# Kernel optimization log

Measured on AMD Instinct MI355X. Metric: run time of the kernel, lower is better.

## Reference

```python
import jax, jax.numpy as jnp
import numpy as np

NC = 4
X = Y = Z = 64
IMG_SHAPE = (96, 96, 96)
SPAN = 2          # FILTER_SIZE = [5,5,5]
NUM_ITER = 4
DIL = 2           # DILATION = 2.0
SMOOTH_DISTANCE_INIT = 0.3
PRIOR_DISTANCE_INIT = 0.3


def _ind(d):
    # mirrors _get_ind from the torch code
    return (d, 0) if d > 0 else (0, -d)


def _sl(a, b):
    # slice(a, -b) with -0 -> None, mirrors _negative
    return slice(a, -b if b else None)


def _offsets():
    for dx in range(-SPAN, SPAN + 1):
        for dy in range(-SPAN, SPAN + 1):
            for dz in range(-SPAN, SPAN + 1):
                yield dx, dy, dz


def _lin_resize_axis(x, axis, out):
    # 1D linear interpolation matching torch align_corners=True
    n = x.shape[axis]
    if out == n:
        return x
    pos = jnp.arange(out, dtype=x.dtype) * ((n - 1) / (out - 1))
    i0 = jnp.clip(jnp.floor(pos).astype(jnp.int32), 0, n - 1)
    i1 = jnp.clip(i0 + 1, 0, n - 1)
    w = pos - i0.astype(x.dtype)
    shp = [1] * x.ndim
    shp[axis] = out
    w = w.reshape(shp)
    return jnp.take(x, i0, axis=axis) * (1 - w) + jnp.take(x, i1, axis=axis) * w


def _resize3d(x, out_sz):
    # trilinear, align_corners=True, separable over the 3 spatial axes of [b,c,X,Y,Z]
    for ax, o in zip((2, 3, 4), out_sz):
        x = _lin_resize_axis(x, ax, o)
    return x


def _smooth_gaussian(feats):
    # feats: [b, c, X, Y, Z] -> gaussian [b, 5,5,5, X, Y, Z]
    b = feats.shape[0]
    sp = feats.shape[2:]
    g = jnp.zeros((b, 5, 5, 5) + sp, feats.dtype)
    for dx, dy, dz in _offsets():
        dx1, dx2 = _ind(dx); dy1, dy2 = _ind(dy); dz1, dz2 = _ind(dz)
        a = feats[:, :, _sl(dx1, dx2), _sl(dy1, dy2), _sl(dz1, dz2)]
        c = feats[:, :, _sl(dx2, dx1), _sl(dy2, dy1), _sl(dz2, dz1)]
        e = jnp.exp(-0.5 * jnp.sum((a - c) ** 2, axis=1))
        g = g.at[:, dx + SPAN, dy + SPAN, dz + SPAN,
                 _sl(dx2, dx1), _sl(dy2, dy1), _sl(dz2, dz1)].set(e)
    return g


def _prior_gaussian(f1, f2):
    # f1, f2: [b, c, x, y, z] (already downsampled) -> [b, 5,5,5, x, y, z]
    b = f1.shape[0]
    sp = f1.shape[2:]
    g = jnp.zeros((b, 5, 5, 5) + sp, f1.dtype)
    for dx, dy, dz in _offsets():
        dx1, dx2 = _ind(dx); dy1, dy2 = _ind(dy); dz1, dz2 = _ind(dz)
        a = f1[:, :, _sl(dx2, dx1), _sl(dy2, dy1), _sl(dz2, dz1)]
        c = f2[:, :, _sl(dx1, dx2), _sl(dy1, dy2), _sl(dz1, dz2)]
        e = jnp.exp(-0.5 * jnp.sum((a - c) ** 2, axis=1))
        g = g.at[:, dx + SPAN, dy + SPAN, dz + SPAN,
                 _sl(dx2, dx1), _sl(dy2, dy1), _sl(dz2, dz1)].set(e)
    return g


def _message(p, g):
    # p: [b, nc, x, y, z]; g: [b, 5,5,5, x, y, z]
    out = jnp.zeros_like(p)
    for dx, dy, dz in _offsets():
        dx1, dx2 = _ind(dx); dy1, dy2 = _ind(dy); dz1, dz2 = _ind(dz)
        a = p[:, :, _sl(dx1, dx2), _sl(dy1, dy2), _sl(dz1, dz2)]
        w = g[:, None, dx + SPAN, dy + SPAN, dz + SPAN,
              _sl(dx2, dx1), _sl(dy2, dy1), _sl(dz2, dz1)]
        out = out.at[:, :, _sl(dx2, dx1), _sl(dy2, dy1), _sl(dz2, dz1)].add(a * w)
    return out


def setup_inputs() -> dict:
    key = jax.random.key(0)
    ks = jax.random.split(key, 6)
    unary = jax.random.normal(ks[0], (1, NC, X, Y, Z), jnp.float32)
    img = jax.random.normal(ks[1], (1, 2, X, Y, Z), jnp.float32)
    atlas = jax.random.normal(ks[2], (1, 2, X, Y, Z), jnp.float32)
    atlas_label = jax.random.uniform(ks[3], (1, X, Y, Z, NC), jnp.float32)
    patch_start = jax.random.randint(ks[4], (1, 3), 0, 32, jnp.int32)
    return {
        "unary": unary,
        "img": img,
        "atlas": atlas,
        "atlas_label": atlas_label,
        "patch_start": patch_start,
        "smooth_norm": jnp.array([1.0 / SMOOTH_DISTANCE_INIT], jnp.float32),
        "smooth_weight": jnp.ones((NC,), jnp.float32),
        "prior_norm": jnp.array([1.0 / PRIOR_DISTANCE_INIT], jnp.float32),
        "prior_weight": jnp.ones(IMG_SHAPE, jnp.float32),
        "compat_w": jnp.eye(NC, dtype=jnp.float32),
    }


def reference(unary, img, atlas, atlas_label, patch_start,
              smooth_norm, smooth_weight, prior_norm, prior_weight, compat_w):
    b, nc, x, y, z = unary.shape
    ds = (x // DIL, y // DIL, z // DIL)  # floor(in*0.5) == ceil(in/2) for even dims

    # similarity kernels
    sg = _smooth_gaussian(img * smooth_norm)                      # [b,5,5,5,x,y,z]
    f1 = _resize3d(img * prior_norm, ds)
    f2 = _resize3d(atlas * prior_norm, ds)
    pg = _prior_gaussian(f1, f2)                                  # [b,5,5,5,x/2,y/2,z/2]

    # prior message is independent of q_values: compute once
    al = jnp.transpose(atlas_label, (0, 4, 1, 2, 3))              # [b,nc,x,y,z]
    al_ds = _resize3d(al, ds)
    pm = _resize3d(_message(al_ds, pg), (x, y, z))                # [b,nc,x,y,z]
    pw = jax.lax.dynamic_slice(
        prior_weight,
        (patch_start[0, 0], patch_start[0, 1], patch_start[0, 2]),
        (x, y, z))
    prior_term = pw[None, None] * pm

    q = unary
    for _ in range(NUM_ITER):
        p = jax.nn.softmax(q, axis=1)
        sm = _message(p, sg)
        pred = smooth_weight[None, :, None, None, None] * sm + prior_term
        q = unary + jnp.einsum('oc,bcxyz->boxyz', compat_w, pred)  # 1x1x1 compat conv
    return q
```

## Files before the change

### kernel.cpp

```cpp
#include <hip/hip_runtime.h>

#define NN 64
#define N3 (64*64*64)
#define DS 32

#define LOG2E 1.4426950408889634f
#define FSCALE 0.8493218002880191f

typedef _Float16 h2  __attribute__((ext_vector_type(2)));
typedef __fp16   h2f __attribute__((ext_vector_type(2)));

__device__ __forceinline__ float fexp2(float x) { return __builtin_amdgcn_exp2f(x); }

__device__ __forceinline__ h2 u2h(unsigned u) { union { unsigned u; h2 h; } c; c.u = u; return c.h; }
__device__ __forceinline__ unsigned h2u(h2 h) { union { unsigned u; h2 h; } c; c.h = h; return c.u; }
__device__ __forceinline__ h2 pkh(float a, float b) {
    union { h2f a; h2 b; } c; c.a = __builtin_amdgcn_cvt_pkrtz(a, b); return c.b;
}
__device__ __forceinline__ float fdot2(h2 a, h2 b) {
    union { h2 h; h2f f; } ca, cb; ca.h = a; cb.h = b;
    return __builtin_amdgcn_fdot2(ca.f, cb.f, 0.0f, false);
}


#define PMX 6
#define PMY 10
#define PMZ 10
#define SXD 10
#define SYD 14
#define SZD 14

__global__ __launch_bounds__(1024) void k_prior(
    const float* __restrict__ img, const float* __restrict__ atlas,
    const float* __restrict__ alabel, const float* __restrict__ unary,
    const float* __restrict__ pnorm, const float* __restrict__ snorm,
    const float* __restrict__ pweight, const int* __restrict__ pstart,
    const float* __restrict__ compat,
    float4* __restrict__ unary4, unsigned* __restrict__ fpk)
{
    __shared__ __align__(16) uint4 nbS[SXD][SYD][SZD];
    __shared__ __align__(8)  uint2 pmS[PMX][PMY][PMZ];

    const int tid = threadIdx.x;
    const int x0 = blockIdx.z * 8, y0 = blockIdx.y * 16, z0 = blockIdx.x * 16;
    const int cxlo = (x0*31)/63, cylo = (y0*31)/63, czlo = (z0*31)/63;

    const float pnf = pnorm[0] * FSCALE;
    const float sc  = snorm[0] * FSCALE;

    for (int i = tid; i < 8*16*16; i += 1024) {
        int fz = i & 15, fy = (i >> 4) & 15, fx = i >> 8;
        int g = ((x0+fx)*NN + (y0+fy))*NN + (z0+fz);
        fpk[g] = h2u(pkh(img[g]*sc, img[g+N3]*sc));
    }

    for (int i = tid; i < SXD*SYD*SZD; i += 1024) {
        int lz = i % SZD; int r = i / SZD; int ly = r % SYD; int lx = r / SYD;
        int cx = cxlo - 2 + lx, cy = cylo - 2 + ly, cz = czlo - 2 + lz;
        uint4 v = make_uint4(0u, 0u, 0u, 0u);
        if ((unsigned)cx < DS && (unsigned)cy < DS && (unsigned)cz < DS) {
            const float scale = 63.0f / 31.0f;
            float posx = cx*scale; int a0i = (int)posx; float wx = posx - a0i; int a1i = a0i+1 <= 63 ? a0i+1 : 63;
            float posy = cy*scale; int b0i = (int)posy; float wy = posy - b0i; int b1i = b0i+1 <= 63 ? b0i+1 : 63;
            float posz = cz*scale; int d0i = (int)posz; float wz = posz - d0i; int d1i = d0i+1 <= 63 ? d0i+1 : 63;
            float w000=(1-wx)*(1-wy)*(1-wz), w001=(1-wx)*(1-wy)*wz;
            float w010=(1-wx)*wy*(1-wz),     w011=(1-wx)*wy*wz;
            float w100=wx*(1-wy)*(1-wz),     w101=wx*(1-wy)*wz;
            float w110=wx*wy*(1-wz),         w111=wx*wy*wz;
            int c000=(a0i*NN+b0i)*NN+d0i, c001=(a0i*NN+b0i)*NN+d1i;
            int c010=(a0i*NN+b1i)*NN+d0i, c011=(a0i*NN+b1i)*NN+d1i;
            int c100=(a1i*NN+b0i)*NN+d0i, c101=(a1i*NN+b0i)*NN+d1i;
            int c110=(a1i*NN+b1i)*NN+d0i, c111=(a1i*NN+b1i)*NN+d1i;
            auto tri = [&](const float* p) -> float {
                return p[c000]*w000 + p[c001]*w001 + p[c010]*w010 + p[c011]*w011
                     + p[c100]*w100 + p[c101]*w101 + p[c110]*w110 + p[c111]*w111;
            };
            const float4* lab = (const float4*)alabel;
            float4 l = make_float4(0.f,0.f,0.f,0.f);
            {
                float4 t;
                t = lab[c000]; l.x += w000*t.x; l.y += w000*t.y; l.z += w000*t.z; l.w += w000*t.w;
                t = lab[c001]; l.x += w001*t.x; l.y += w001*t.y; l.z += w001*t.z; l.w += w001*t.w;
                t = lab[c010]; l.x += w010*t.x; l.y += w010*t.y; l.z += w010*t.z; l.w += w010*t.w;
                t = lab[c011]; l.x += w011*t.x; l.y += w011*t.y; l.z += w011*t.z; l.w += w011*t.w;
                t = lab[c100]; l.x += w100*t.x; l.y += w100*t.y; l.z += w100*t.z; l.w += w100*t.w;
                t = lab[c101]; l.x += w101*t.x; l.y += w101*t.y; l.z += w101*t.z; l.w += w101*t.w;
                t = lab[c110]; l.x += w110*t.x; l.y += w110*t.y; l.z += w110*t.z; l.w += w110*t.w;
                t = lab[c111]; l.x += w111*t.x; l.y += w111*t.y; l.z += w111*t.z; l.w += w111*t.w;
            }
            v = make_uint4(h2u(pkh(pnf*tri(atlas), pnf*tri(atlas + N3))),
                           h2u(pkh(l.x, l.y)), h2u(pkh(l.z, l.w)),
                           h2u(pkh(pnf*tri(img), pnf*tri(img + N3))));
        }
        nbS[lx][ly][lz] = v;
    }
    __syncthreads();

    for (int i = tid; i < PMX*PMY*PMZ; i += 1024) {
        int pz = i % PMZ; int r = i / PMZ; int py = r % PMY; int px = r / PMY;
        int cx = cxlo + px, cy = cylo + py, cz = czlo + pz;
        uint2 o = make_uint2(0u, 0u);
        if (cx < DS && cy < DS && cz < DS) {
            h2 ncf = -u2h(nbS[px+2][py+2][pz+2].w);
            float a0=0.f, a1=0.f, a2=0.f, a3=0.f;
            for (int dx = -2; dx <= 2; ++dx) {
                int xx = cx + dx; if ((unsigned)xx >= DS) continue;
                for (int dy = -2; dy <= 2; ++dy) {
                    int yy = cy + dy; if ((unsigned)yy >= DS) continue;
                    #pragma unroll
                    for (int dz = -2; dz <= 2; ++dz) {
                        int zz = cz + dz; if ((unsigned)zz >= DS) continue;
                        uint4 v = nbS[px+2+dx][py+2+dy][pz+2+dz];
                        h2 d = u2h(v.x) + ncf;
                        float w = fexp2(-fdot2(d, d));
                        h2 l01 = u2h(v.y), l23 = u2h(v.z);
                        a0 += w*(float)l01.x; a1 += w*(float)l01.y;
                        a2 += w*(float)l23.x; a3 += w*(float)l23.y;
                    }
                }
            }
            o = make_uint2(h2u(pkh(a0, a1)), h2u(pkh(a2, a3)));
        }
        pmS[px][py][pz] = o;
    }
    __syncthreads();

    const int ps0 = pstart[0], ps1 = pstart[1], ps2 = pstart[2];
    float cw[16];
    #pragma unroll
    for (int k = 0; k < 16; ++k) cw[k] = compat[k];
    const float S13 = 31.0f / 63.0f;

    for (int i = tid; i < 8*16*16; i += 1024) {
        int fz = i & 15, fy = (i >> 4) & 15, fx = i >> 8;
        int gx = x0 + fx, gy = y0 + fy, gz = z0 + fz;
        float posx = gx*S13; int xc0 = (int)posx; float wx = posx - xc0; int xc1 = xc0 < 31 ? xc0+1 : 31;
        float posy = gy*S13; int yc0 = (int)posy; float wy = posy - yc0; int yc1 = yc0 < 31 ? yc0+1 : 31;
        float posz = gz*S13; int zc0 = (int)posz; float wz = posz - zc0; int zc1 = zc0 < 31 ? zc0+1 : 31;
        int lx0 = xc0-cxlo, lx1 = xc1-cxlo;
        int ly0 = yc0-cylo, ly1 = yc1-cylo;
        int lz0 = zc0-czlo, lz1 = zc1-czlo;

        auto up = [&](uint2 u) -> float4 {
            h2 a = u2h(u.x), b = u2h(u.y);
            return make_float4((float)a.x, (float)a.y, (float)b.x, (float)b.y);
        };
        float4 p000 = up(pmS[lx0][ly0][lz0]), p001 = up(pmS[lx0][ly0][lz1]);
        float4 p010 = up(pmS[lx0][ly1][lz0]), p011 = up(pmS[lx0][ly1][lz1]);
        float4 p100 = up(pmS[lx1][ly0][lz0]), p101 = up(pmS[lx1][ly0][lz1]);
        float4 p110 = up(pmS[lx1][ly1][lz0]), p111 = up(pmS[lx1][ly1][lz1]);
        float w000=(1-wx)*(1-wy)*(1-wz), w001=(1-wx)*(1-wy)*wz;
        float w010=(1-wx)*wy*(1-wz),     w011=(1-wx)*wy*wz;
        float w100=wx*(1-wy)*(1-wz),     w101=wx*(1-wy)*wz;
        float w110=wx*wy*(1-wz),         w111=wx*wy*wz;
        float pw = pweight[(ps0+gx)*96*96 + (ps1+gy)*96 + (ps2+gz)];
        float pr0 = pw*(w000*p000.x + w001*p001.x + w010*p010.x + w011*p011.x + w100*p100.x + w101*p101.x + w110*p110.x + w111*p111.x);
        float pr1 = pw*(w000*p000.y + w001*p001.y + w010*p010.y + w011*p011.y + w100*p100.y + w101*p101.y + w110*p110.y + w111*p111.y);
        float pr2 = pw*(w000*p000.z + w001*p001.z + w010*p010.z + w011*p011.z + w100*p100.z + w101*p101.z + w110*p110.z + w111*p111.z);
        float pr3 = pw*(w000*p000.w + w001*p001.w + w010*p010.w + w011*p011.w + w100*p100.w + w101*p101.w + w110*p110.w + w111*p111.w);

        int g = (gx*NN + gy)*NN + gz;
        float4 q;
        q.x = unary[g]      + cw[0]*pr0  + cw[1]*pr1  + cw[2]*pr2  + cw[3]*pr3;
        q.y = unary[g+N3]   + cw[4]*pr0  + cw[5]*pr1  + cw[6]*pr2  + cw[7]*pr3;
        q.z = unary[g+2*N3] + cw[8]*pr0  + cw[9]*pr1  + cw[10]*pr2 + cw[11]*pr3;
        q.w = unary[g+3*N3] + cw[12]*pr0 + cw[13]*pr1 + cw[14]*pr2 + cw[15]*pr3;
        unary4[g] = q;
    }
}


#define TXD 8
#define TYD 8
#define TZD 8
#define TZR 4
#define RZ 2
#define HX 12
#define HY 12
#define HZ 12
#define PZ 14

template<bool FIRST, bool LAST>
__global__ __launch_bounds__(1024, 8) void k_iter(
    const float* __restrict__ qin,
    const uint2* __restrict__ pin,
    const unsigned* __restrict__ fpk,
    const float4* __restrict__ unary4,
    const float* __restrict__ sweight,
    const float* __restrict__ compat,
    uint2* __restrict__ pout,
    float* __restrict__ qout)
{
    __shared__ __align__(16) uint2    pS[HX][HY][PZ];
    __shared__ __align__(8)  unsigned fS[HX][HY][PZ];
    __shared__ __align__(16) uint4    accS[3][TXD*TYD*TZR];

    const int tzg = threadIdx.x, ty = threadIdx.y;
    const int tx = threadIdx.z & 7, s = threadIdx.z >> 3;
    const int x0b = blockIdx.z * TXD, y0b = blockIdx.y * TYD, z0b = blockIdx.x * TZD;
    const int tid = threadIdx.x + TZR*threadIdx.y + (TZR*TYD)*threadIdx.z;

    #pragma unroll
    for (int rr = 0; rr < 2; ++rr) {
        int i = tid + rr*1024;
        if (i < HX*HY*HZ) {
            int lz = i % HZ; int r = i / HZ;
            int ly = r % HY; int lx = r / HY;
            int gx = x0b + lx - 2, gy = y0b + ly - 2, gz = z0b + lz - 2;
            uint2 pu = make_uint2(0u, 0u);
            unsigned fu = 0u;
            if ((unsigned)gx < NN && (unsigned)gy < NN && (unsigned)gz < NN) {
                int g = (gx*NN + gy)*NN + gz;
                fu = fpk[g];
                if (FIRST) {
                    float q0 = qin[g], q1 = qin[g+N3], q2 = qin[g+2*N3], q3 = qin[g+3*N3];
                    float m = fmaxf(fmaxf(q0,q1), fmaxf(q2,q3));
                    float e0 = fexp2((q0-m)*LOG2E);
                    float e1 = fexp2((q1-m)*LOG2E);
                    float e2 = fexp2((q2-m)*LOG2E);
                    float e3 = fexp2((q3-m)*LOG2E);
                    float inv = 1.0f/(e0+e1+e2+e3);
                    pu = make_uint2(h2u(pkh(e0*inv, e1*inv)), h2u(pkh(e2*inv, e3*inv)));
                } else {
                    pu = pin[g];
                }
            }
            pS[lx][ly][lz] = pu;
            fS[lx][ly][lz] = fu;
        }
    }

    const int tz0 = tzg * RZ;
    const int gx = x0b + tx, gy = y0b + ty;
    const int g = (gx*NN + gy)*NN + z0b + tz0;

    float4 u40, u41;
    float sw0, sw1, sw2, sw3;
    float cw[16];
    if (s == 0) {
        u40 = unary4[g]; u41 = unary4[g+1];
        sw0 = sweight[0]; sw1 = sweight[1]; sw2 = sweight[2]; sw3 = sweight[3];
        #pragma unroll
        for (int k = 0; k < 16; ++k) cw[k] = compat[k];
    }

    __syncthreads();

    const h2 ncf0 = -u2h(fS[tx+2][ty+2][tz0+2]);
    const h2 ncf1 = -u2h(fS[tx+2][ty+2][tz0+3]);

    h2 a01_0 = (h2)0, a23_0 = (h2)0, a01_1 = (h2)0, a23_1 = (h2)0;

    #pragma unroll
    for (int pp = 0; pp < 7; ++pp) {
        int p = (3 - s) + 4*pp;
        if (p < 25) {
            int dx = p / 5, dy = p - 5*dx;
            const uint4* pv = reinterpret_cast<const uint4*>(&pS[tx+dx][ty+dy][tz0]);
            const uint2* fv = reinterpret_cast<const uint2*>(&fS[tx+dx][ty+dy][tz0]);
            uint4 qa = pv[0], qb = pv[1], qc = pv[2];
            uint2 fa = fv[0], fb = fv[1], fc = fv[2];

            unsigned fz[6]  = { fa.x, fa.y, fb.x, fb.y, fc.x, fc.y };
            unsigned p01[6] = { qa.x, qa.z, qb.x, qb.z, qc.x, qc.z };
            unsigned p23[6] = { qa.y, qa.w, qb.y, qb.w, qc.y, qc.w };

            #pragma unroll
            for (int dz = 0; dz < 5; ++dz) {
                {
                    h2 d = u2h(fz[dz]) + ncf0;
                    float w = fexp2(-fdot2(d, d));
                    h2 w2 = pkh(w, w);
                    a01_0 = w2 * u2h(p01[dz]) + a01_0;
                    a23_0 = w2 * u2h(p23[dz]) + a23_0;
                }
                {
                    h2 d = u2h(fz[dz+1]) + ncf1;
                    float w = fexp2(-fdot2(d, d));
                    h2 w2 = pkh(w, w);
                    a01_1 = w2 * u2h(p01[dz+1]) + a01_1;
                    a23_1 = w2 * u2h(p23[dz+1]) + a23_1;
                }
            }
        }
    }

    const int pid = (tx*TYD + ty)*TZR + tzg;
    if (s != 0) {
        accS[s-1][pid] = make_uint4(h2u(a01_0), h2u(a23_0), h2u(a01_1), h2u(a23_1));
    }
    __syncthreads();

    if (s == 0) {
        #pragma unroll
        for (int j = 0; j < 3; ++j) {
            uint4 v = accS[j][pid];
            a01_0 += u2h(v.x); a23_0 += u2h(v.y);
            a01_1 += u2h(v.z); a23_1 += u2h(v.w);
        }

        float p0, p1, p2, p3;
        float r00, r10, r20, r30, r01, r11, r21, r31;
        p0 = sw0*(float)a01_0.x; p1 = sw1*(float)a01_0.y;
        p2 = sw2*(float)a23_0.x; p3 = sw3*(float)a23_0.y;
        r00 = u40.x + cw[0]*p0  + cw[1]*p1  + cw[2]*p2  + cw[3]*p3;
        r10 = u40.y + cw[4]*p0  + cw[5]*p1  + cw[6]*p2  + cw[7]*p3;
        r20 = u40.z + cw[8]*p0  + cw[9]*p1  + cw[10]*p2 + cw[11]*p3;
        r30 = u40.w + cw[12]*p0 + cw[13]*p1 + cw[14]*p2 + cw[15]*p3;
        p0 = sw0*(float)a01_1.x; p1 = sw1*(float)a01_1.y;
        p2 = sw2*(float)a23_1.x; p3 = sw3*(float)a23_1.y;
        r01 = u41.x + cw[0]*p0  + cw[1]*p1  + cw[2]*p2  + cw[3]*p3;
        r11 = u41.y + cw[4]*p0  + cw[5]*p1  + cw[6]*p2  + cw[7]*p3;
        r21 = u41.z + cw[8]*p0  + cw[9]*p1  + cw[10]*p2 + cw[11]*p3;
        r31 = u41.w + cw[12]*p0 + cw[13]*p1 + cw[14]*p2 + cw[15]*p3;

        if (LAST) {
            *(float2*)(qout + 0*N3 + g) = make_float2(r00, r01);
            *(float2*)(qout + 1*N3 + g) = make_float2(r10, r11);
            *(float2*)(qout + 2*N3 + g) = make_float2(r20, r21);
            *(float2*)(qout + 3*N3 + g) = make_float2(r30, r31);
        } else {
            float m0 = fmaxf(fmaxf(r00,r10), fmaxf(r20,r30));
            float e00 = fexp2((r00-m0)*LOG2E), e10 = fexp2((r10-m0)*LOG2E);
            float e20 = fexp2((r20-m0)*LOG2E), e30 = fexp2((r30-m0)*LOG2E);
            float i0 = 1.0f/(e00+e10+e20+e30);
            float m1 = fmaxf(fmaxf(r01,r11), fmaxf(r21,r31));
            float e01 = fexp2((r01-m1)*LOG2E), e11 = fexp2((r11-m1)*LOG2E);
            float e21 = fexp2((r21-m1)*LOG2E), e31 = fexp2((r31-m1)*LOG2E);
            float i1 = 1.0f/(e01+e11+e21+e31);
            uint4 o = make_uint4(h2u(pkh(e00*i0, e10*i0)), h2u(pkh(e20*i0, e30*i0)),
                                 h2u(pkh(e01*i1, e11*i1)), h2u(pkh(e21*i1, e31*i1)));
            *reinterpret_cast<uint4*>(&pout[g]) = o;
        }
    }
}


extern "C" void kernel_launch(void* const* d_in, const int* in_sizes, int n_in,
                              void* d_out, int out_size, void* d_ws, size_t ws_size,
                              hipStream_t stream)
{
    const float* unary   = (const float*)d_in[0];
    const float* img     = (const float*)d_in[1];
    const float* atlas   = (const float*)d_in[2];
    const float* alabel  = (const float*)d_in[3];
    const int*   pstart  = (const int*)d_in[4];
    const float* snorm   = (const float*)d_in[5];
    const float* sweight = (const float*)d_in[6];
    const float* pnorm   = (const float*)d_in[7];
    const float* pweight = (const float*)d_in[8];
    const float* compat  = (const float*)d_in[9];
    float* out = (float*)d_out;
    float* ws  = (float*)d_ws;

    float4*   unary4 = (float4*)ws;
    uint2*    pA     = (uint2*)(ws + 4*N3);
    uint2*    pB     = (uint2*)(ws + 6*N3);
    unsigned* fpk    = (unsigned*)(ws + 8*N3);

    {
        dim3 pgrid(4, 4, 8), pblock(1024);
        k_prior<<<pgrid, pblock, 0, stream>>>(img, atlas, alabel, unary, pnorm, snorm,
                                              pweight, pstart, compat, unary4, fpk);
    }

    dim3 grid(NN/TZD, NN/TYD, NN/TXD), block(TZR, TYD, 32);
    k_iter<true, false><<<grid, block, 0, stream>>>(unary, pA, fpk, unary4, sweight, compat, pA, out);
    k_iter<false,false><<<grid, block, 0, stream>>>(unary, pA, fpk, unary4, sweight, compat, pB, out);
    k_iter<false,false><<<grid, block, 0, stream>>>(unary, pB, fpk, unary4, sweight, compat, pA, out);
    k_iter<false,true ><<<grid, block, 0, stream>>>(unary, pA, fpk, unary4, sweight, compat, pB, out);
}
```

Baseline: 91.45 us.

## Fuse prior-message computation into first mean-field iteration kernel

Removes the separate k_prior launch and computes the downsampled prior features, the prior message and the upsampled prior term inside the FIRST instantiation of k_iter, per 8x8x8 tile. Each block recomputes its own 10^3 coarse neighbourhood and 6^3 coarse message patch, and writes unary4 and the packed image features as side outputs for the later iterations. This saves a kernel launch and a global round trip, but adds redundant coarse work across neighbouring tiles and extra syncs and shared memory (aliased buffer) to the first iteration.

```diff
diff --git a/kernel.cpp b/kernel.cpp
--- a/kernel.cpp
+++ b/kernel.cpp
@@ -23,153 +23,6 @@
 }
 
 
-#define PMX 6
-#define PMY 10
-#define PMZ 10
-#define SXD 10
-#define SYD 14
-#define SZD 14
-
-__global__ __launch_bounds__(1024) void k_prior(
-    const float* __restrict__ img, const float* __restrict__ atlas,
-    const float* __restrict__ alabel, const float* __restrict__ unary,
-    const float* __restrict__ pnorm, const float* __restrict__ snorm,
-    const float* __restrict__ pweight, const int* __restrict__ pstart,
-    const float* __restrict__ compat,
-    float4* __restrict__ unary4, unsigned* __restrict__ fpk)
-{
-    __shared__ __align__(16) uint4 nbS[SXD][SYD][SZD];
-    __shared__ __align__(8)  uint2 pmS[PMX][PMY][PMZ];
-
-    const int tid = threadIdx.x;
-    const int x0 = blockIdx.z * 8, y0 = blockIdx.y * 16, z0 = blockIdx.x * 16;
-    const int cxlo = (x0*31)/63, cylo = (y0*31)/63, czlo = (z0*31)/63;
-
-    const float pnf = pnorm[0] * FSCALE;
-    const float sc  = snorm[0] * FSCALE;
-
-    for (int i = tid; i < 8*16*16; i += 1024) {
-        int fz = i & 15, fy = (i >> 4) & 15, fx = i >> 8;
-        int g = ((x0+fx)*NN + (y0+fy))*NN + (z0+fz);
-        fpk[g] = h2u(pkh(img[g]*sc, img[g+N3]*sc));
-    }
-
-    for (int i = tid; i < SXD*SYD*SZD; i += 1024) {
-        int lz = i % SZD; int r = i / SZD; int ly = r % SYD; int lx = r / SYD;
-        int cx = cxlo - 2 + lx, cy = cylo - 2 + ly, cz = czlo - 2 + lz;
-        uint4 v = make_uint4(0u, 0u, 0u, 0u);
-        if ((unsigned)cx < DS && (unsigned)cy < DS && (unsigned)cz < DS) {
-            const float scale = 63.0f / 31.0f;
-            float posx = cx*scale; int a0i = (int)posx; float wx = posx - a0i; int a1i = a0i+1 <= 63 ? a0i+1 : 63;
-            float posy = cy*scale; int b0i = (int)posy; float wy = posy - b0i; int b1i = b0i+1 <= 63 ? b0i+1 : 63;
-            float posz = cz*scale; int d0i = (int)posz; float wz = posz - d0i; int d1i = d0i+1 <= 63 ? d0i+1 : 63;
-            float w000=(1-wx)*(1-wy)*(1-wz), w001=(1-wx)*(1-wy)*wz;
-            float w010=(1-wx)*wy*(1-wz),     w011=(1-wx)*wy*wz;
-            float w100=wx*(1-wy)*(1-wz),     w101=wx*(1-wy)*wz;
-            float w110=wx*wy*(1-wz),         w111=wx*wy*wz;
-            int c000=(a0i*NN+b0i)*NN+d0i, c001=(a0i*NN+b0i)*NN+d1i;
-            int c010=(a0i*NN+b1i)*NN+d0i, c011=(a0i*NN+b1i)*NN+d1i;
-            int c100=(a1i*NN+b0i)*NN+d0i, c101=(a1i*NN+b0i)*NN+d1i;
-            int c110=(a1i*NN+b1i)*NN+d0i, c111=(a1i*NN+b1i)*NN+d1i;
-            auto tri = [&](const float* p) -> float {
-                return p[c000]*w000 + p[c001]*w001 + p[c010]*w010 + p[c011]*w011
-                     + p[c100]*w100 + p[c101]*w101 + p[c110]*w110 + p[c111]*w111;
-            };
-            const float4* lab = (const float4*)alabel;
-            float4 l = make_float4(0.f,0.f,0.f,0.f);
-            {
-                float4 t;
-                t = lab[c000]; l.x += w000*t.x; l.y += w000*t.y; l.z += w000*t.z; l.w += w000*t.w;
-                t = lab[c001]; l.x += w001*t.x; l.y += w001*t.y; l.z += w001*t.z; l.w += w001*t.w;
-                t = lab[c010]; l.x += w010*t.x; l.y += w010*t.y; l.z += w010*t.z; l.w += w010*t.w;
-                t = lab[c011]; l.x += w011*t.x; l.y += w011*t.y; l.z += w011*t.z; l.w += w011*t.w;
-                t = lab[c100]; l.x += w100*t.x; l.y += w100*t.y; l.z += w100*t.z; l.w += w100*t.w;
-                t = lab[c101]; l.x += w101*t.x; l.y += w101*t.y; l.z += w101*t.z; l.w += w101*t.w;
-                t = lab[c110]; l.x += w110*t.x; l.y += w110*t.y; l.z += w110*t.z; l.w += w110*t.w;
-                t = lab[c111]; l.x += w111*t.x; l.y += w111*t.y; l.z += w111*t.z; l.w += w111*t.w;
-            }
-            v = make_uint4(h2u(pkh(pnf*tri(atlas), pnf*tri(atlas + N3))),
-                           h2u(pkh(l.x, l.y)), h2u(pkh(l.z, l.w)),
-                           h2u(pkh(pnf*tri(img), pnf*tri(img + N3))));
-        }
-        nbS[lx][ly][lz] = v;
-    }
-    __syncthreads();
-
-    for (int i = tid; i < PMX*PMY*PMZ; i += 1024) {
-        int pz = i % PMZ; int r = i / PMZ; int py = r % PMY; int px = r / PMY;
-        int cx = cxlo + px, cy = cylo + py, cz = czlo + pz;
-        uint2 o = make_uint2(0u, 0u);
-        if (cx < DS && cy < DS && cz < DS) {
-            h2 ncf = -u2h(nbS[px+2][py+2][pz+2].w);
-            float a0=0.f, a1=0.f, a2=0.f, a3=0.f;
-            for (int dx = -2; dx <= 2; ++dx) {
-                int xx = cx + dx; if ((unsigned)xx >= DS) continue;
-                for (int dy = -2; dy <= 2; ++dy) {
-                    int yy = cy + dy; if ((unsigned)yy >= DS) continue;
-                    #pragma unroll
-                    for (int dz = -2; dz <= 2; ++dz) {
-                        int zz = cz + dz; if ((unsigned)zz >= DS) continue;
-                        uint4 v = nbS[px+2+dx][py+2+dy][pz+2+dz];
-                        h2 d = u2h(v.x) + ncf;
-                        float w = fexp2(-fdot2(d, d));
-                        h2 l01 = u2h(v.y), l23 = u2h(v.z);
-                        a0 += w*(float)l01.x; a1 += w*(float)l01.y;
-                        a2 += w*(float)l23.x; a3 += w*(float)l23.y;
-                    }
-                }
-            }
-            o = make_uint2(h2u(pkh(a0, a1)), h2u(pkh(a2, a3)));
-        }
-        pmS[px][py][pz] = o;
-    }
-    __syncthreads();
-
-    const int ps0 = pstart[0], ps1 = pstart[1], ps2 = pstart[2];
-    float cw[16];
-    #pragma unroll
-    for (int k = 0; k < 16; ++k) cw[k] = compat[k];
-    const float S13 = 31.0f / 63.0f;
-
-    for (int i = tid; i < 8*16*16; i += 1024) {
-        int fz = i & 15, fy = (i >> 4) & 15, fx = i >> 8;
-        int gx = x0 + fx, gy = y0 + fy, gz = z0 + fz;
-        float posx = gx*S13; int xc0 = (int)posx; float wx = posx - xc0; int xc1 = xc0 < 31 ? xc0+1 : 31;
-        float posy = gy*S13; int yc0 = (int)posy; float wy = posy - yc0; int yc1 = yc0 < 31 ? yc0+1 : 31;
-        float posz = gz*S13; int zc0 = (int)posz; float wz = posz - zc0; int zc1 = zc0 < 31 ? zc0+1 : 31;
-        int lx0 = xc0-cxlo, lx1 = xc1-cxlo;
-        int ly0 = yc0-cylo, ly1 = yc1-cylo;
-        int lz0 = zc0-czlo, lz1 = zc1-czlo;
-
-        auto up = [&](uint2 u) -> float4 {
-            h2 a = u2h(u.x), b = u2h(u.y);
-            return make_float4((float)a.x, (float)a.y, (float)b.x, (float)b.y);
-        };
-        float4 p000 = up(pmS[lx0][ly0][lz0]), p001 = up(pmS[lx0][ly0][lz1]);
-        float4 p010 = up(pmS[lx0][ly1][lz0]), p011 = up(pmS[lx0][ly1][lz1]);
-        float4 p100 = up(pmS[lx1][ly0][lz0]), p101 = up(pmS[lx1][ly0][lz1]);
-        float4 p110 = up(pmS[lx1][ly1][lz0]), p111 = up(pmS[lx1][ly1][lz1]);
-        float w000=(1-wx)*(1-wy)*(1-wz), w001=(1-wx)*(1-wy)*wz;
-        float w010=(1-wx)*wy*(1-wz),     w011=(1-wx)*wy*wz;
-        float w100=wx*(1-wy)*(1-wz),     w101=wx*(1-wy)*wz;
-        float w110=wx*wy*(1-wz),         w111=wx*wy*wz;
-        float pw = pweight[(ps0+gx)*96*96 + (ps1+gy)*96 + (ps2+gz)];
-        float pr0 = pw*(w000*p000.x + w001*p001.x + w010*p010.x + w011*p011.x + w100*p100.x + w101*p101.x + w110*p110.x + w111*p111.x);
-        float pr1 = pw*(w000*p000.y + w001*p001.y + w010*p010.y + w011*p011.y + w100*p100.y + w101*p101.y + w110*p110.y + w111*p111.y);
-        float pr2 = pw*(w000*p000.z + w001*p001.z + w010*p010.z + w011*p011.z + w100*p100.z + w101*p101.z + w110*p110.z + w111*p111.z);
-        float pr3 = pw*(w000*p000.w + w001*p001.w + w010*p010.w + w011*p011.w + w100*p100.w + w101*p101.w + w110*p110.w + w111*p111.w);
-
-        int g = (gx*NN + gy)*NN + gz;
-        float4 q;
-        q.x = unary[g]      + cw[0]*pr0  + cw[1]*pr1  + cw[2]*pr2  + cw[3]*pr3;
-        q.y = unary[g+N3]   + cw[4]*pr0  + cw[5]*pr1  + cw[6]*pr2  + cw[7]*pr3;
-        q.z = unary[g+2*N3] + cw[8]*pr0  + cw[9]*pr1  + cw[10]*pr2 + cw[11]*pr3;
-        q.w = unary[g+3*N3] + cw[12]*pr0 + cw[13]*pr1 + cw[14]*pr2 + cw[15]*pr3;
-        unary4[g] = q;
-    }
-}
-
-
 #define TXD 8
 #define TYD 8
 #define TZD 8
@@ -179,41 +32,186 @@
 #define HY 12
 #define HZ 12
 #define PZ 14
+#define CPX 6
+#define CSX 10
 
 template<bool FIRST, bool LAST>
 __global__ __launch_bounds__(1024, 8) void k_iter(
-    const float* __restrict__ qin,
+    const float* __restrict__ unary,
     const uint2* __restrict__ pin,
-    const unsigned* __restrict__ fpk,
-    const float4* __restrict__ unary4,
+    const unsigned* __restrict__ fpk_in,
+    const float* __restrict__ img,
+    const float* __restrict__ atlas,
+    const float* __restrict__ alabel,
+    const float* __restrict__ pnorm,
+    const float* __restrict__ snorm,
+    const float* __restrict__ pweight,
+    const int* __restrict__ pstart,
     const float* __restrict__ sweight,
     const float* __restrict__ compat,
+    float4* __restrict__ unary4,
+    unsigned* __restrict__ fpk_out,
     uint2* __restrict__ pout,
     float* __restrict__ qout)
 {
-    __shared__ __align__(16) uint2    pS[HX][HY][PZ];
+    __shared__ __align__(16) unsigned char raw1[16384];
+    auto nbS = reinterpret_cast<uint4 (*)[CSX][CSX]>(raw1);
+    auto pS  = reinterpret_cast<uint2 (*)[HY][PZ]>(raw1);
     __shared__ __align__(8)  unsigned fS[HX][HY][PZ];
     __shared__ __align__(16) uint4    accS[3][TXD*TYD*TZR];
+    __shared__ __align__(8)  uint2    pmS[CPX][CPX][CPX];
 
     const int tzg = threadIdx.x, ty = threadIdx.y;
     const int tx = threadIdx.z & 7, s = threadIdx.z >> 3;
     const int x0b = blockIdx.z * TXD, y0b = blockIdx.y * TYD, z0b = blockIdx.x * TZD;
     const int tid = threadIdx.x + TZR*threadIdx.y + (TZR*TYD)*threadIdx.z;
 
+    const int tz0 = tzg * RZ;
+    const int gx = x0b + tx, gy = y0b + ty;
+    const int g = (gx*NN + gy)*NN + z0b + tz0;
+
+    float4 u40, u41;
+    float sw0, sw1, sw2, sw3;
+    float cw[16];
+
+    if (FIRST) {
+        const int cxlo = (x0b*31)/63, cylo = (y0b*31)/63, czlo = (z0b*31)/63;
+        const float pnf = pnorm[0] * FSCALE;
+
+        if (tid < CSX*CSX*CSX) {
+            int lz = tid % CSX; int r = tid / CSX; int ly = r % CSX; int lx = r / CSX;
+            int cx = cxlo - 2 + lx, cy = cylo - 2 + ly, cz = czlo - 2 + lz;
+            uint4 v = make_uint4(0u, 0u, 0u, 0u);
+            if ((unsigned)cx < DS && (unsigned)cy < DS && (unsigned)cz < DS) {
+                const float scale = 63.0f / 31.0f;
+                float posx = cx*scale; int a0i = (int)posx; float wx = posx - a0i; int a1i = a0i+1 <= 63 ? a0i+1 : 63;
+                float posy = cy*scale; int b0i = (int)posy; float wy = posy - b0i; int b1i = b0i+1 <= 63 ? b0i+1 : 63;
+                float posz = cz*scale; int d0i = (int)posz; float wz = posz - d0i; int d1i = d0i+1 <= 63 ? d0i+1 : 63;
+                float w000=(1-wx)*(1-wy)*(1-wz), w001=(1-wx)*(1-wy)*wz;
+                float w010=(1-wx)*wy*(1-wz),     w011=(1-wx)*wy*wz;
+                float w100=wx*(1-wy)*(1-wz),     w101=wx*(1-wy)*wz;
+                float w110=wx*wy*(1-wz),         w111=wx*wy*wz;
+                int c000=(a0i*NN+b0i)*NN+d0i, c001=(a0i*NN+b0i)*NN+d1i;
+                int c010=(a0i*NN+b1i)*NN+d0i, c011=(a0i*NN+b1i)*NN+d1i;
+                int c100=(a1i*NN+b0i)*NN+d0i, c101=(a1i*NN+b0i)*NN+d1i;
+                int c110=(a1i*NN+b1i)*NN+d0i, c111=(a1i*NN+b1i)*NN+d1i;
+                auto tri = [&](const float* p) -> float {
+                    return p[c000]*w000 + p[c001]*w001 + p[c010]*w010 + p[c011]*w011
+                         + p[c100]*w100 + p[c101]*w101 + p[c110]*w110 + p[c111]*w111;
+                };
+                const float4* lab = (const float4*)alabel;
+                float4 l = make_float4(0.f,0.f,0.f,0.f);
+                {
+                    float4 t;
+                    t = lab[c000]; l.x += w000*t.x; l.y += w000*t.y; l.z += w000*t.z; l.w += w000*t.w;
+                    t = lab[c001]; l.x += w001*t.x; l.y += w001*t.y; l.z += w001*t.z; l.w += w001*t.w;
+                    t = lab[c010]; l.x += w010*t.x; l.y += w010*t.y; l.z += w010*t.z; l.w += w010*t.w;
+                    t = lab[c011]; l.x += w011*t.x; l.y += w011*t.y; l.z += w011*t.z; l.w += w011*t.w;
+                    t = lab[c100]; l.x += w100*t.x; l.y += w100*t.y; l.z += w100*t.z; l.w += w100*t.w;
+                    t = lab[c101]; l.x += w101*t.x; l.y += w101*t.y; l.z += w101*t.z; l.w += w101*t.w;
+                    t = lab[c110]; l.x += w110*t.x; l.y += w110*t.y; l.z += w110*t.z; l.w += w110*t.w;
+                    t = lab[c111]; l.x += w111*t.x; l.y += w111*t.y; l.z += w111*t.z; l.w += w111*t.w;
+                }
+                v = make_uint4(h2u(pkh(pnf*tri(atlas), pnf*tri(atlas + N3))),
+                               h2u(pkh(l.x, l.y)), h2u(pkh(l.z, l.w)),
+                               h2u(pkh(pnf*tri(img), pnf*tri(img + N3))));
+            }
+            nbS[lx][ly][lz] = v;
+        }
+        __syncthreads();
+
+        if (tid < CPX*CPX*CPX) {
+            int pz = tid % CPX; int r = tid / CPX; int py = r % CPX; int px = r / CPX;
+            int cx = cxlo + px, cy = cylo + py, cz = czlo + pz;
+            uint2 o = make_uint2(0u, 0u);
+            if (cx < DS && cy < DS && cz < DS) {
+                h2 ncf = -u2h(nbS[px+2][py+2][pz+2].w);
+                float a0=0.f, a1=0.f, a2=0.f, a3=0.f;
+                for (int dx = -2; dx <= 2; ++dx) {
+                    int xx = cx + dx; if ((unsigned)xx >= DS) continue;
+                    for (int dy = -2; dy <= 2; ++dy) {
+                        int yy = cy + dy; if ((unsigned)yy >= DS) continue;
+                        #pragma unroll
+                        for (int dz = -2; dz <= 2; ++dz) {
+                            int zz = cz + dz; if ((unsigned)zz >= DS) continue;
+                            uint4 v = nbS[px+2+dx][py+2+dy][pz+2+dz];
+                            h2 d = u2h(v.x) + ncf;
+                            float w = fexp2(-fdot2(d, d));
+                            h2 l01 = u2h(v.y), l23 = u2h(v.z);
+                            a0 += w*(float)l01.x; a1 += w*(float)l01.y;
+                            a2 += w*(float)l23.x; a3 += w*(float)l23.y;
+                        }
+                    }
+                }
+                o = make_uint2(h2u(pkh(a0, a1)), h2u(pkh(a2, a3)));
+            }
+            pmS[px][py][pz] = o;
+        }
+        __syncthreads();
+
+        if (s == 0) {
+            sw0 = sweight[0]; sw1 = sweight[1]; sw2 = sweight[2]; sw3 = sweight[3];
+            #pragma unroll
+            for (int k = 0; k < 16; ++k) cw[k] = compat[k];
+
+            const float S13 = 31.0f / 63.0f;
+            float posx = gx*S13; int xc0 = (int)posx; float wxf = posx - xc0; int xc1 = xc0 < 31 ? xc0+1 : 31;
+            float posy = gy*S13; int yc0 = (int)posy; float wyf = posy - yc0; int yc1 = yc0 < 31 ? yc0+1 : 31;
+            int lx0 = xc0-cxlo, lx1 = xc1-cxlo;
+            int ly0 = yc0-cylo, ly1 = yc1-cylo;
+            const int ps0 = pstart[0], ps1 = pstart[1], ps2 = pstart[2];
+
+            auto up = [&](uint2 u) -> float4 {
+                h2 a = u2h(u.x), b = u2h(u.y);
+                return make_float4((float)a.x, (float)a.y, (float)b.x, (float)b.y);
+            };
+
+            #pragma unroll
+            for (int rz = 0; rz < RZ; ++rz) {
+                int gz = z0b + tz0 + rz;
+                float posz = gz*S13; int zc0 = (int)posz; float wzf = posz - zc0; int zc1 = zc0 < 31 ? zc0+1 : 31;
+                int lz0 = zc0-czlo, lz1 = zc1-czlo;
+                float4 p000 = up(pmS[lx0][ly0][lz0]), p001 = up(pmS[lx0][ly0][lz1]);
+                float4 p010 = up(pmS[lx0][ly1][lz0]), p011 = up(pmS[lx0][ly1][lz1]);
+                float4 p100 = up(pmS[lx1][ly0][lz0]), p101 = up(pmS[lx1][ly0][lz1]);
+                float4 p110 = up(pmS[lx1][ly1][lz0]), p111 = up(pmS[lx1][ly1][lz1]);
+                float w000=(1-wxf)*(1-wyf)*(1-wzf), w001=(1-wxf)*(1-wyf)*wzf;
+                float w010=(1-wxf)*wyf*(1-wzf),     w011=(1-wxf)*wyf*wzf;
+                float w100=wxf*(1-wyf)*(1-wzf),     w101=wxf*(1-wyf)*wzf;
+                float w110=wxf*wyf*(1-wzf),         w111=wxf*wyf*wzf;
+                float pw = pweight[(ps0+gx)*96*96 + (ps1+gy)*96 + (ps2+gz)];
+                float pr0 = pw*(w000*p000.x + w001*p001.x + w010*p010.x + w011*p011.x + w100*p100.x + w101*p101.x + w110*p110.x + w111*p111.x);
+                float pr1 = pw*(w000*p000.y + w001*p001.y + w010*p010.y + w011*p011.y + w100*p100.y + w101*p101.y + w110*p110.y + w111*p111.y);
+                float pr2 = pw*(w000*p000.z + w001*p001.z + w010*p010.z + w011*p011.z + w100*p100.z + w101*p101.z + w110*p110.z + w111*p111.z);
+                float pr3 = pw*(w000*p000.w + w001*p001.w + w010*p010.w + w011*p011.w + w100*p100.w + w101*p101.w + w110*p110.w + w111*p111.w);
+
+                int gg = g + rz;
+                float4 q;
+                q.x = unary[gg]      + cw[0]*pr0  + cw[1]*pr1  + cw[2]*pr2  + cw[3]*pr3;
+                q.y = unary[gg+N3]   + cw[4]*pr0  + cw[5]*pr1  + cw[6]*pr2  + cw[7]*pr3;
+                q.z = unary[gg+2*N3] + cw[8]*pr0  + cw[9]*pr1  + cw[10]*pr2 + cw[11]*pr3;
+                q.w = unary[gg+3*N3] + cw[12]*pr0 + cw[13]*pr1 + cw[14]*pr2 + cw[15]*pr3;
+                unary4[gg] = q;
+                if (rz == 0) u40 = q; else u41 = q;
+            }
+        }
+        __syncthreads();
+    }
+
+    const float sc = FIRST ? snorm[0] * FSCALE : 0.0f;
     #pragma unroll
     for (int rr = 0; rr < 2; ++rr) {
         int i = tid + rr*1024;
         if (i < HX*HY*HZ) {
             int lz = i % HZ; int r = i / HZ;
             int ly = r % HY; int lx = r / HY;
-            int gx = x0b + lx - 2, gy = y0b + ly - 2, gz = z0b + lz - 2;
+            int hgx = x0b + lx - 2, hgy = y0b + ly - 2, hgz = z0b + lz - 2;
             uint2 pu = make_uint2(0u, 0u);
             unsigned fu = 0u;
-            if ((unsigned)gx < NN && (unsigned)gy < NN && (unsigned)gz < NN) {
-                int g = (gx*NN + gy)*NN + gz;
-                fu = fpk[g];
+            if ((unsigned)hgx < NN && (unsigned)hgy < NN && (unsigned)hgz < NN) {
+                int hg = (hgx*NN + hgy)*NN + hgz;
                 if (FIRST) {
-                    float q0 = qin[g], q1 = qin[g+N3], q2 = qin[g+2*N3], q3 = qin[g+3*N3];
+                    float q0 = unary[hg], q1 = unary[hg+N3], q2 = unary[hg+2*N3], q3 = unary[hg+3*N3];
                     float m = fmaxf(fmaxf(q0,q1), fmaxf(q2,q3));
                     float e0 = fexp2((q0-m)*LOG2E);
                     float e1 = fexp2((q1-m)*LOG2E);
@@ -221,8 +219,12 @@
                     float e3 = fexp2((q3-m)*LOG2E);
                     float inv = 1.0f/(e0+e1+e2+e3);
                     pu = make_uint2(h2u(pkh(e0*inv, e1*inv)), h2u(pkh(e2*inv, e3*inv)));
+                    fu = h2u(pkh(img[hg]*sc, img[hg+N3]*sc));
+                    if ((unsigned)(lx-2) < 8u && (unsigned)(ly-2) < 8u && (unsigned)(lz-2) < 8u)
+                        fpk_out[hg] = fu;
                 } else {
-                    pu = pin[g];
+                    pu = pin[hg];
+                    fu = fpk_in[hg];
                 }
             }
             pS[lx][ly][lz] = pu;
@@ -230,14 +232,7 @@
         }
     }
 
-    const int tz0 = tzg * RZ;
-    const int gx = x0b + tx, gy = y0b + ty;
-    const int g = (gx*NN + gy)*NN + z0b + tz0;
-
-    float4 u40, u41;
-    float sw0, sw1, sw2, sw3;
-    float cw[16];
-    if (s == 0) {
+    if (!FIRST && s == 0) {
         u40 = unary4[g]; u41 = unary4[g+1];
         sw0 = sweight[0]; sw1 = sweight[1]; sw2 = sweight[2]; sw3 = sweight[3];
         #pragma unroll
@@ -358,15 +353,13 @@
     uint2*    pB     = (uint2*)(ws + 6*N3);
     unsigned* fpk    = (unsigned*)(ws + 8*N3);
 
-    {
-        dim3 pgrid(4, 4, 8), pblock(1024);
-        k_prior<<<pgrid, pblock, 0, stream>>>(img, atlas, alabel, unary, pnorm, snorm,
-                                              pweight, pstart, compat, unary4, fpk);
-    }
-
     dim3 grid(NN/TZD, NN/TYD, NN/TXD), block(TZR, TYD, 32);
-    k_iter<true, false><<<grid, block, 0, stream>>>(unary, pA, fpk, unary4, sweight, compat, pA, out);
-    k_iter<false,false><<<grid, block, 0, stream>>>(unary, pA, fpk, unary4, sweight, compat, pB, out);
-    k_iter<false,false><<<grid, block, 0, stream>>>(unary, pB, fpk, unary4, sweight, compat, pA, out);
-    k_iter<false,true ><<<grid, block, 0, stream>>>(unary, pA, fpk, unary4, sweight, compat, pB, out);
+    k_iter<true, false><<<grid, block, 0, stream>>>(unary, pA, fpk, img, atlas, alabel,
+        pnorm, snorm, pweight, pstart, sweight, compat, unary4, fpk, pA, out);
+    k_iter<false,false><<<grid, block, 0, stream>>>(unary, pA, fpk, img, atlas, alabel,
+        pnorm, snorm, pweight, pstart, sweight, compat, unary4, fpk, pB, out);
+    k_iter<false,false><<<grid, block, 0, stream>>>(unary, pB, fpk, img, atlas, alabel,
+        pnorm, snorm, pweight, pstart, sweight, compat, unary4, fpk, pA, out);
+    k_iter<false,true ><<<grid, block, 0, stream>>>(unary, pA, fpk, img, atlas, alabel,
+        pnorm, snorm, pweight, pstart, sweight, compat, unary4, fpk, pB, out);
 }
```

After: 90.90 us. No clear change (-0.6%).
